# Kernel optimization log

Measured on AMD Instinct MI355X. Metric: run time of the kernel, lower is better.

Reference implementation:

```python
import jax, jax.numpy as jnp
import numpy as np
import math

EMBED = 1024
HEADS = 16
HEAD_DIM = EMBED // HEADS


def setup_inputs() -> dict:
    key = jax.random.key(0)
    ks = jax.random.split(key, 9)
    B, S = 2, 2048
    query = jax.random.normal(ks[0], (B, S, EMBED), dtype=jnp.float32)
    key_t = jax.random.normal(ks[1], (B, S, EMBED), dtype=jnp.float32)
    value = jax.random.normal(ks[2], (B, S, EMBED), dtype=jnp.float32)
    mask = jax.random.randint(ks[3], (B, 1, S, S), 0, 2, dtype=jnp.int32)
    # nn.Linear(head_dim, head_dim, bias=False) weights: [out, in]
    sc = 1.0 / math.sqrt(HEAD_DIM)
    Wq = jax.random.uniform(ks[4], (HEAD_DIM, HEAD_DIM), jnp.float32, -sc, sc)
    Wk = jax.random.uniform(ks[5], (HEAD_DIM, HEAD_DIM), jnp.float32, -sc, sc)
    Wv = jax.random.uniform(ks[6], (HEAD_DIM, HEAD_DIM), jnp.float32, -sc, sc)
    so = 1.0 / math.sqrt(EMBED)
    Wo = jax.random.uniform(ks[7], (EMBED, EMBED), jnp.float32, -so, so)
    bo = jax.random.uniform(ks[8], (EMBED,), jnp.float32, -so, so)
    return {"query": query, "key": key_t, "value": value, "mask": mask,
            "Wq": Wq, "Wk": Wk, "Wv": Wv, "Wo": Wo, "bo": bo}


def reference(query, key, value, mask, Wq, Wk, Wv, Wo, bo):
    B, Sq, E = query.shape
    Sk = key.shape[1]
    H, D = HEADS, HEAD_DIM
    # Faithful raw reshape into heads (as in the torch source, no transpose)
    q = query.reshape(B, H, Sq, D)
    k = key.reshape(B, H, Sk, D)
    v = value.reshape(B, H, Sk, D)
    # per-head_dim Linear (bias-free): x @ W.T
    Q = jnp.einsum('bhsd,ed->bhse', q, Wq)
    K = jnp.einsum('bhsd,ed->bhse', k, Wk)
    V = jnp.einsum('bhsd,ed->bhse', v, Wv)
    scores = jnp.einsum('bhqd,bhkd->bhqk', Q, K)  # [B,H,Sq,Sk]
    scores = jnp.where(mask == 0, jnp.float32(-1e20), scores)
    # NOTE: source divides by sqrt(embed_size), not sqrt(head_dim)
    attn = jax.nn.softmax(scores / jnp.float32(math.sqrt(E)), axis=-1)
    out = jnp.einsum('bhqk,bhkd->bhqd', attn, V).reshape(B, Sq, H * D)
    return out @ Wo.T + bo
```

## Files before the change

kernel.cpp:

```cpp
#include <hip/hip_runtime.h>

typedef __attribute__((ext_vector_type(8))) short short8;
typedef __attribute__((ext_vector_type(4))) float f32x4;
typedef __attribute__((ext_vector_type(2))) int int2v;
typedef __attribute__((ext_vector_type(4))) int int4v;

__device__ __forceinline__ short f2bf(float f) {
  unsigned u = __builtin_bit_cast(unsigned, f);
  u += 0x7fff + ((u >> 16) & 1);
  return (short)(u >> 16);
}

__device__ __forceinline__ int pk2bf(float lo, float hi) {
#if defined(__gfx950__) && __has_builtin(__builtin_amdgcn_cvt_pk_bf16_f32)
  typedef __attribute__((ext_vector_type(2))) __bf16 bf16x2;
  bf16x2 v = __builtin_amdgcn_cvt_pk_bf16_f32(lo, hi);
  return __builtin_bit_cast(int, v);
#else
  return (int)(unsigned short)(short)f2bf(lo) | (((int)f2bf(hi)) << 16);
#endif
}

__device__ __forceinline__ int pktr(float lo, float hi) {
  return (int)(__builtin_bit_cast(unsigned, lo) >> 16) |
         (int)(__builtin_bit_cast(unsigned, hi) & 0xffff0000u);
}

__device__ __forceinline__ short8 pack8(f32x4 a, f32x4 b) {
  int4v t;
  t.x = pk2bf(a[0], a[1]);
  t.y = pk2bf(a[2], a[3]);
  t.z = pk2bf(b[0], b[1]);
  t.w = pk2bf(b[2], b[3]);
  return __builtin_bit_cast(short8, t);
}

__device__ __forceinline__ float fand(float p, int m) {
  return __builtin_bit_cast(float, __builtin_bit_cast(int, p) & m);
}

__device__ __forceinline__ int bmask(unsigned w, int bit) {
#if __has_builtin(__builtin_amdgcn_sbfe)
  return __builtin_amdgcn_sbfe((int)w, bit, 1);
#else
  return ((int)(w << (31 - bit))) >> 31;
#endif
}

__device__ __forceinline__ float fexp2(float x) {
#if __has_builtin(__builtin_amdgcn_exp2f)
  return __builtin_amdgcn_exp2f(x);
#else
  return exp2f(x);
#endif
}

__device__ __forceinline__ void glds16(const short* g, short* lbase, int lane) {
#if __has_builtin(__builtin_amdgcn_global_load_lds)
  __builtin_amdgcn_global_load_lds(
      (const __attribute__((address_space(1))) unsigned int*)g,
      (__attribute__((address_space(3))) unsigned int*)lbase, 16, 0, 0);
#else
  *(short8*)(lbase + lane * 8) = *(const short8*)g;
#endif
}

__global__ __launch_bounds__(256) void prep(const float* __restrict__ q,
                                            const float* __restrict__ k,
                                            const float* __restrict__ v,
                                            const float* __restrict__ Wq,
                                            const float* __restrict__ Wk,
                                            const float* __restrict__ Wv,
                                            const float* __restrict__ Wo,
                                            const int* __restrict__ mask,
                                            short* __restrict__ Qp,
                                            short* __restrict__ Kp,
                                            short* __restrict__ Vtp,
                                            short* __restrict__ Wob,
                                            unsigned* __restrict__ mmod) {
  const int bid = blockIdx.x;
  const int tid = threadIdx.x;

  if (bid >= 4096) {
    const int mb = bid - 4096;
    const int kp = mb & 15, bq = mb >> 4;
    const int b_ = bq >> 5, q64 = bq & 31;
    const int wv = tid >> 6, qd = (tid >> 4) & 3, m16_ = tid & 15;
    unsigned d = 0;
#pragma unroll
    for (int hb = 0; hb < 2; ++hb) {
      const int ka = kp * 2 + hb;
#pragma unroll
      for (int r = 0; r < 4; ++r) {
        const int* mr = mask + b_ * 4194304 +
                        (q64 * 64 + wv * 16 + qd * 4 + r) * 2048 + ka * 64 + m16_;
#pragma unroll
        for (int nt = 0; nt < 4; ++nt)
          if (mr[nt * 16] != 0) d |= 1u << (hb * 16 + r * 4 + nt);
      }
    }
    mmod[mb * 256 + tid] = d;
    return;
  }
  if (bid >= 3072) {
    const int i = ((bid - 3072) * 256 + tid) * 4;
    const f32x4 x = *(const f32x4*)&Wo[i];
    int2v o;
    o.x = pk2bf(x[0], x[1]);
    o.y = pk2bf(x[2], x[3]);
    *(int2v*)&Wob[i] = o;
    return;
  }

  __shared__ short xt[64][72];
  __shared__ short ot[64][72];
  const int mode = bid >> 10;
  const int bt = bid & 1023;
  const float* X;
  const float* W;
  float scale;
  if (mode == 0) { X = q; W = Wq; scale = 0.045084220f; }
  else if (mode == 1) { X = k; W = Wk; scale = 1.0f; }
  else { X = v; W = Wv; scale = 1.0f; }

  const int r0 = bt * 64;
  const int row = tid >> 2, seg = (tid & 3) * 16;
  const f32x4* xs = (const f32x4*)(X + (r0 + row) * 64 + seg);
  const f32x4 x0 = xs[0], x1 = xs[1], x2 = xs[2], x3 = xs[3];
  *(short8*)&xt[row][seg] = pack8(x0, x1);
  *(short8*)&xt[row][seg + 8] = pack8(x2, x3);
  __syncthreads();

  const int lane = tid & 63, wave = tid >> 6;
  const int m16 = lane & 15, quad = lane >> 4;

  const short8 a0 = *(const short8*)&xt[wave * 16 + m16][quad * 8];
  const short8 a1 = *(const short8*)&xt[wave * 16 + m16][32 + quad * 8];

  f32x4 acc[4];
#pragma unroll
  for (int nt = 0; nt < 4; ++nt) {
    const f32x4* wp0 = (const f32x4*)&W[(nt * 16 + m16) * 64 + quad * 8];
    const f32x4* wp1 = (const f32x4*)&W[(nt * 16 + m16) * 64 + 32 + quad * 8];
    const short8 b0 = pack8(wp0[0], wp0[1]);
    const short8 b1 = pack8(wp1[0], wp1[1]);
    f32x4 z = (f32x4){0.f, 0.f, 0.f, 0.f};
    z = __builtin_amdgcn_mfma_f32_16x16x32_bf16(a0, b0, z, 0, 0, 0);
    z = __builtin_amdgcn_mfma_f32_16x16x32_bf16(a1, b1, z, 0, 0, 0);
    acc[nt] = z;
  }

  if (mode != 2) {
#pragma unroll
    for (int nt = 0; nt < 4; ++nt)
#pragma unroll
      for (int r = 0; r < 4; ++r)
        ot[wave * 16 + quad * 4 + r][nt * 16 + m16] = f2bf(acc[nt][r] * scale);
  } else {
#pragma unroll
    for (int nt = 0; nt < 4; ++nt)
#pragma unroll
      for (int r = 0; r < 4; ++r)
        ot[nt * 16 + m16][16 * quad + 4 * r + wave] = f2bf(acc[nt][r]);
  }
  __syncthreads();

  const int orow = tid >> 2, opart = tid & 3;
  if (mode != 2) {
    short* dst = (mode == 0 ? Qp : Kp) + (r0 + orow) * 64 + opart * 16;
    *(short8*)&dst[0] = *(const short8*)&ot[orow][opart * 16];
    *(short8*)&dst[8] = *(const short8*)&ot[orow][opart * 16 + 8];
  } else {
    const int bh = r0 >> 11, s0 = r0 & 2047;
    short* dst = Vtp + bh * 131072 + orow * 2048 + s0 + opart * 16;
    *(short8*)&dst[0] = *(const short8*)&ot[orow][opart * 16];
    *(short8*)&dst[8] = *(const short8*)&ot[orow][opart * 16 + 8];
  }
}

__global__ __launch_bounds__(256) void flash64f(const short* __restrict__ Qp,
                                                const short* __restrict__ Kp,
                                                const short* __restrict__ Vt,
                                                const unsigned* __restrict__ mmod,
                                                short* __restrict__ Ob) {
  __shared__ __attribute__((aligned(16))) short kt0[4096];
  __shared__ __attribute__((aligned(16))) short kt1[4096];
  __shared__ __attribute__((aligned(16))) short vt0[4096];
  __shared__ __attribute__((aligned(16))) short vt1[4096];
  __shared__ __attribute__((aligned(16))) short pt[4096];
  const int tid = threadIdx.x;
  const int bid = blockIdx.x;
  const int local = bid >> 3;
  const int qblk = local & 31;
  const int bh = (bid & 7) * 4 + (local >> 5);
  const int q0 = qblk << 6;
  const int b = bh >> 4;
  const short* Qh = Qp + bh * 131072;
  const short* Kh = Kp + bh * 131072;
  const short* Vh = Vt + bh * 131072;
  const int lane = tid & 63, wave = tid >> 6;
  const int m16 = lane & 15, quad = lane >> 4;
  const int srow = lane >> 3, sj = (lane & 7) ^ srow;
  const int koff = m16 * 128 + ((quad ^ (m16 & 7)) * 16);
  const unsigned* mq = mmod + ((b * 32 + qblk) * 16) * 256 + tid;

  char* const ptB = (char*)pt;
  int woff[4];
#pragma unroll
  for (int r = 0; r < 4; ++r)
    woff[r] = (wave * 16 + quad * 4 + r) * 128 +
              ((m16 * 8) ^ (((quad * 4 + r) & 7) << 4));
  const int aswz = (m16 & 7) << 4;
  const int aoff0 = (wave * 16 + m16) * 128 + ((quad * 16) ^ aswz);
  const int aoff1 = (wave * 16 + m16) * 128 + ((quad * 16 + 64) ^ aswz);

  short8 aq[2];
#pragma unroll
  for (int h = 0; h < 2; ++h)
    aq[h] = *(const short8*)&Qh[(q0 + wave * 16 + m16) * 64 + h * 32 + quad * 8];

  float l[4] = {0.f, 0.f, 0.f, 0.f};
  f32x4 oacc[4];
#pragma unroll
  for (int dt = 0; dt < 4; ++dt) oacc[dt] = (f32x4){0.f, 0.f, 0.f, 0.f};

  auto stage = [&](short* ktb, short* vtb, int ka) {
#pragma unroll
    for (int t = 0; t < 2; ++t) {
      const int crow = wave * 16 + t * 8;
      glds16(Kh + (ka * 64 + crow + srow) * 64 + sj * 8, ktb + crow * 64, lane);
      glds16(Vh + (crow + srow) * 2048 + ka * 64 + sj * 8, vtb + crow * 64, lane);
    }
  };

  auto compute = [&](const short* ktp, const short* vtp, unsigned mw, int bitbase) {
    const char* ktb = (const char*)ktp;
    const char* vtb = (const char*)vtp;
    f32x4 s[4];
    __builtin_amdgcn_s_setprio(1);
#pragma unroll
    for (int nt = 0; nt < 4; ++nt) {
      const int o0 = nt * 2048 + koff;
      const short8 kb0 = *(const short8*)(ktb + o0);
      const short8 kb1 = *(const short8*)(ktb + (o0 ^ 64));
      f32x4 z = (f32x4){0.f, 0.f, 0.f, 0.f};
      z = __builtin_amdgcn_mfma_f32_16x16x32_bf16(aq[0], kb0, z, 0, 0, 0);
      z = __builtin_amdgcn_mfma_f32_16x16x32_bf16(aq[1], kb1, z, 0, 0, 0);
      s[nt] = z;
    }
    __builtin_amdgcn_s_setprio(0);

#pragma unroll
    for (int r = 0; r < 4; ++r) {
      float p[4];
#pragma unroll
      for (int nt = 0; nt < 4; ++nt)
        p[nt] = fand(fexp2(s[nt][r]), bmask(mw, bitbase + r * 4 + nt));
      l[r] += (p[0] + p[1]) + (p[2] + p[3]);
      int2v pp;
      pp.x = pktr(p[0], p[1]);
      pp.y = pktr(p[2], p[3]);
      *(int2v*)(ptB + woff[r]) = pp;
    }

    const short8 ap0 = *(const short8*)(ptB + aoff0);
    const short8 ap1 = *(const short8*)(ptB + aoff1);
    __builtin_amdgcn_s_setprio(1);
#pragma unroll
    for (int dt = 0; dt < 4; ++dt) {
      const int o0 = dt * 2048 + koff;
      const short8 vb0 = *(const short8*)(vtb + o0);
      const short8 vb1 = *(const short8*)(vtb + (o0 ^ 64));
      f32x4 z = oacc[dt];
      z = __builtin_amdgcn_mfma_f32_16x16x32_bf16(ap0, vb0, z, 0, 0, 0);
      z = __builtin_amdgcn_mfma_f32_16x16x32_bf16(ap1, vb1, z, 0, 0, 0);
      oacc[dt] = z;
    }
    __builtin_amdgcn_s_setprio(0);
  };

  unsigned mw = mq[0];
  stage(kt0, vt0, 0);
  asm volatile("s_waitcnt vmcnt(0)" ::: "memory");
  __builtin_amdgcn_s_barrier();

  for (int kk = 0; kk < 16; ++kk) {
    stage(kt1, vt1, 2 * kk + 1);
    compute(kt0, vt0, mw, 0);
    asm volatile("s_waitcnt vmcnt(0)" ::: "memory");
    __builtin_amdgcn_s_barrier();

    unsigned mwn = 0u;
    if (kk < 15) {
      mwn = mq[(kk + 1) * 256];
      stage(kt0, vt0, 2 * kk + 2);
    }
    compute(kt1, vt1, mw, 16);
    mw = mwn;
    if (kk < 15) {
      asm volatile("s_waitcnt vmcnt(0)" ::: "memory");
      __builtin_amdgcn_s_barrier();
    }
  }

#pragma unroll
  for (int r = 0; r < 4; ++r) {
#pragma unroll
    for (int off = 1; off < 16; off <<= 1) l[r] += __shfl_xor(l[r], off, 16);
    const float inv = 1.0f / l[r];
#pragma unroll
    for (int dt = 0; dt < 4; ++dt)
      *(short*)(ptB + (wave * 16 + quad * 4 + r) * 128 +
                ((dt * 32 + m16 * 2) ^ (((quad * 4 + r) & 7) << 4))) =
          f2bf(oacc[dt][r] * inv);
  }

  const int orow = lane >> 2, opart = lane & 3;
  const int prow = wave * 16 + orow;
  const int oswz = (orow & 7) << 4;
  short* og = Ob + (bh * 2048 + q0 + prow) * 64 + opart * 16;
  *(short8*)&og[0] = *(const short8*)(ptB + prow * 128 + ((opart * 32) ^ oswz));
  *(short8*)&og[8] = *(const short8*)(ptB + prow * 128 + ((opart * 32 + 16) ^ oswz));
}

__global__ __launch_bounds__(256) void outproj(const short* __restrict__ Ob,
                                               const short* __restrict__ Wob,
                                               const float* __restrict__ bo,
                                               float* __restrict__ out) {
  __shared__ short at[64][72];
  __shared__ short bt[128][72];
  const int tid = threadIdx.x;
  const int bid = blockIdx.x;
  const int ct = bid >> 6, rt = bid & 63;
  const int r0 = rt * 64, c0 = ct * 128;
  const int lane = tid & 63, wave = tid >> 6;
  const int mr = (wave >> 1) * 32, nc = (wave & 1) * 64;
  const int m16 = lane & 15, quad = lane >> 4;
  const int arow = tid >> 2, apart = tid & 3;
  const int brow = tid >> 1, bhalf = (tid & 1) * 32;

  f32x4 acc[2][4];
#pragma unroll
  for (int mt = 0; mt < 2; ++mt)
#pragma unroll
    for (int nt = 0; nt < 4; ++nt) acc[mt][nt] = (f32x4){0.f, 0.f, 0.f, 0.f};

  for (int kc = 0; kc < 16; ++kc) {
    __syncthreads();
    const short* ag = &Ob[(r0 + arow) * 1024 + kc * 64 + apart * 16];
    const short* bg = &Wob[(c0 + brow) * 1024 + kc * 64 + bhalf];
    *(short8*)&at[arow][apart * 16] = *(const short8*)&ag[0];
    *(short8*)&at[arow][apart * 16 + 8] = *(const short8*)&ag[8];
    *(short8*)&bt[brow][bhalf] = *(const short8*)&bg[0];
    *(short8*)&bt[brow][bhalf + 8] = *(const short8*)&bg[8];
    *(short8*)&bt[brow][bhalf + 16] = *(const short8*)&bg[16];
    *(short8*)&bt[brow][bhalf + 24] = *(const short8*)&bg[24];
    __syncthreads();

#pragma unroll
    for (int kh = 0; kh < 2; ++kh) {
      short8 af[2], bf[4];
#pragma unroll
      for (int i = 0; i < 2; ++i)
        af[i] = *(const short8*)&at[mr + i * 16 + m16][kh * 32 + quad * 8];
#pragma unroll
      for (int j = 0; j < 4; ++j)
        bf[j] = *(const short8*)&bt[nc + j * 16 + m16][kh * 32 + quad * 8];
#pragma unroll
      for (int mt = 0; mt < 2; ++mt)
#pragma unroll
        for (int nt = 0; nt < 4; ++nt)
          acc[mt][nt] = __builtin_amdgcn_mfma_f32_16x16x32_bf16(af[mt], bf[nt], acc[mt][nt], 0, 0, 0);
    }
  }

#pragma unroll
  for (int nt = 0; nt < 4; ++nt) {
    const int col = c0 + nc + nt * 16 + m16;
    const float bias = bo[col];
#pragma unroll
    for (int mt = 0; mt < 2; ++mt)
#pragma unroll
      for (int rr2 = 0; rr2 < 4; ++rr2)
        out[(r0 + mr + mt * 16 + quad * 4 + rr2) * 1024 + col] = acc[mt][nt][rr2] + bias;
  }
}

extern "C" void kernel_launch(void* const* d_in, const int* in_sizes, int n_in,
                              void* d_out, int out_size, void* d_ws, size_t ws_size,
                              hipStream_t stream) {
  const float* query = (const float*)d_in[0];
  const float* key = (const float*)d_in[1];
  const float* value = (const float*)d_in[2];
  const int* mask = (const int*)d_in[3];
  const float* Wq = (const float*)d_in[4];
  const float* Wk = (const float*)d_in[5];
  const float* Wv = (const float*)d_in[6];
  const float* Wo = (const float*)d_in[7];
  const float* bo = (const float*)d_in[8];
  float* out = (float*)d_out;

  char* ws = (char*)d_ws;
  short* Qp = (short*)(ws);
  short* Kp = (short*)(ws + 8388608);
  short* Vt = (short*)(ws + 16777216);
  short* Ob = (short*)(ws + 25165824);
  short* Wob = (short*)(ws + 41943040);
  unsigned* mmod = (unsigned*)(ws + 44564480);

  prep<<<5120, 256, 0, stream>>>(query, key, value, Wq, Wk, Wv, Wo, mask,
                                 Qp, Kp, Vt, Wob, mmod);
  flash64f<<<1024, 256, 0, stream>>>(Qp, Kp, Vt, mmod, Ob);
  outproj<<<512, 256, 0, stream>>>(Ob, Wob, bo, out);
}
```

Measured before the change: 229.8 us.

## Process 128 query rows per flash block to reuse staged K/V tiles

The flash attention kernel now handles 128 query rows per workgroup (two 64-row halves per wave) instead of 64, halving the grid to 512 blocks. Each K/V tile staged into LDS therefore feeds twice as many MFMAs, which halves global K/V traffic and LDS staging per unit of work. The pipeline is also restructured: both buffers are prefetched up front and partial vmcnt waits replace full drains. In exchange, register pressure and LDS use rise, and only 512 blocks may underfill a 256-CU device.

```diff
diff --git a/kernel.cpp b/kernel.cpp
--- a/kernel.cpp
+++ b/kernel.cpp
@@ -178,7 +178,7 @@
   }
 }
 
-__global__ __launch_bounds__(256) void flash64f(const short* __restrict__ Qp,
+__global__ __launch_bounds__(256) void flash128(const short* __restrict__ Qp,
                                                 const short* __restrict__ Kp,
                                                 const short* __restrict__ Vt,
                                                 const unsigned* __restrict__ mmod,
@@ -187,13 +187,13 @@
   __shared__ __attribute__((aligned(16))) short kt1[4096];
   __shared__ __attribute__((aligned(16))) short vt0[4096];
   __shared__ __attribute__((aligned(16))) short vt1[4096];
-  __shared__ __attribute__((aligned(16))) short pt[4096];
+  __shared__ __attribute__((aligned(16))) short pt[8192];
   const int tid = threadIdx.x;
   const int bid = blockIdx.x;
   const int local = bid >> 3;
-  const int qblk = local & 31;
-  const int bh = (bid & 7) * 4 + (local >> 5);
-  const int q0 = qblk << 6;
+  const int qblk = local & 15;
+  const int bh = (bid & 7) * 4 + (local >> 4);
+  const int q0 = qblk << 7;
   const int b = bh >> 4;
   const short* Qh = Qp + bh * 131072;
   const short* Kh = Kp + bh * 131072;
@@ -202,27 +202,36 @@
   const int m16 = lane & 15, quad = lane >> 4;
   const int srow = lane >> 3, sj = (lane & 7) ^ srow;
   const int koff = m16 * 128 + ((quad ^ (m16 & 7)) * 16);
-  const unsigned* mq = mmod + ((b * 32 + qblk) * 16) * 256 + tid;
+  const unsigned* mqa = mmod + ((b * 32 + qblk * 2) * 16) * 256 + tid;
 
   char* const ptB = (char*)pt;
-  int woff[4];
-#pragma unroll
-  for (int r = 0; r < 4; ++r)
-    woff[r] = (wave * 16 + quad * 4 + r) * 128 +
-              ((m16 * 8) ^ (((quad * 4 + r) & 7) << 4));
+  int woff[2][4];
+  int aoff[2][2];
   const int aswz = (m16 & 7) << 4;
-  const int aoff0 = (wave * 16 + m16) * 128 + ((quad * 16) ^ aswz);
-  const int aoff1 = (wave * 16 + m16) * 128 + ((quad * 16 + 64) ^ aswz);
-
-  short8 aq[2];
-#pragma unroll
-  for (int h = 0; h < 2; ++h)
-    aq[h] = *(const short8*)&Qh[(q0 + wave * 16 + m16) * 64 + h * 32 + quad * 8];
-
-  float l[4] = {0.f, 0.f, 0.f, 0.f};
-  f32x4 oacc[4];
-#pragma unroll
-  for (int dt = 0; dt < 4; ++dt) oacc[dt] = (f32x4){0.f, 0.f, 0.f, 0.f};
+#pragma unroll
+  for (int mi = 0; mi < 2; ++mi) {
+#pragma unroll
+    for (int r = 0; r < 4; ++r)
+      woff[mi][r] = (mi * 64 + wave * 16 + quad * 4 + r) * 128 +
+                    ((m16 * 8) ^ (((quad * 4 + r) & 7) << 4));
+    aoff[mi][0] = (mi * 64 + wave * 16 + m16) * 128 + ((quad * 16) ^ aswz);
+    aoff[mi][1] = (mi * 64 + wave * 16 + m16) * 128 + (((quad * 16) + 64) ^ aswz);
+  }
+
+  short8 aq[2][2];
+#pragma unroll
+  for (int mi = 0; mi < 2; ++mi)
+#pragma unroll
+    for (int h = 0; h < 2; ++h)
+      aq[mi][h] = *(const short8*)&Qh[(q0 + mi * 64 + wave * 16 + m16) * 64 +
+                                      h * 32 + quad * 8];
+
+  float l[2][4] = {{0.f, 0.f, 0.f, 0.f}, {0.f, 0.f, 0.f, 0.f}};
+  f32x4 oacc[2][4];
+#pragma unroll
+  for (int mi = 0; mi < 2; ++mi)
+#pragma unroll
+    for (int dt = 0; dt < 4; ++dt) oacc[mi][dt] = (f32x4){0.f, 0.f, 0.f, 0.f};
 
   auto stage = [&](short* ktb, short* vtb, int ka) {
 #pragma unroll
@@ -233,94 +242,118 @@
     }
   };
 
-  auto compute = [&](const short* ktp, const short* vtp, unsigned mw, int bitbase) {
+  auto compute = [&](const short* ktp, const short* vtp, unsigned mwa, unsigned mwb,
+                     int bitbase) {
     const char* ktb = (const char*)ktp;
     const char* vtb = (const char*)vtp;
-    f32x4 s[4];
+    f32x4 s[2][4];
     __builtin_amdgcn_s_setprio(1);
 #pragma unroll
     for (int nt = 0; nt < 4; ++nt) {
       const int o0 = nt * 2048 + koff;
       const short8 kb0 = *(const short8*)(ktb + o0);
       const short8 kb1 = *(const short8*)(ktb + (o0 ^ 64));
-      f32x4 z = (f32x4){0.f, 0.f, 0.f, 0.f};
-      z = __builtin_amdgcn_mfma_f32_16x16x32_bf16(aq[0], kb0, z, 0, 0, 0);
-      z = __builtin_amdgcn_mfma_f32_16x16x32_bf16(aq[1], kb1, z, 0, 0, 0);
-      s[nt] = z;
+#pragma unroll
+      for (int mi = 0; mi < 2; ++mi) {
+        f32x4 z = (f32x4){0.f, 0.f, 0.f, 0.f};
+        z = __builtin_amdgcn_mfma_f32_16x16x32_bf16(aq[mi][0], kb0, z, 0, 0, 0);
+        z = __builtin_amdgcn_mfma_f32_16x16x32_bf16(aq[mi][1], kb1, z, 0, 0, 0);
+        s[mi][nt] = z;
+      }
     }
     __builtin_amdgcn_s_setprio(0);
 
 #pragma unroll
-    for (int r = 0; r < 4; ++r) {
-      float p[4];
-#pragma unroll
-      for (int nt = 0; nt < 4; ++nt)
-        p[nt] = fand(fexp2(s[nt][r]), bmask(mw, bitbase + r * 4 + nt));
-      l[r] += (p[0] + p[1]) + (p[2] + p[3]);
-      int2v pp;
-      pp.x = pktr(p[0], p[1]);
-      pp.y = pktr(p[2], p[3]);
-      *(int2v*)(ptB + woff[r]) = pp;
-    }
-
-    const short8 ap0 = *(const short8*)(ptB + aoff0);
-    const short8 ap1 = *(const short8*)(ptB + aoff1);
+    for (int mi = 0; mi < 2; ++mi) {
+      const unsigned mw = mi ? mwb : mwa;
+#pragma unroll
+      for (int r = 0; r < 4; ++r) {
+        float p[4];
+#pragma unroll
+        for (int nt = 0; nt < 4; ++nt)
+          p[nt] = fand(fexp2(s[mi][nt][r]), bmask(mw, bitbase + r * 4 + nt));
+        l[mi][r] += (p[0] + p[1]) + (p[2] + p[3]);
+        int2v pp;
+        pp.x = pktr(p[0], p[1]);
+        pp.y = pktr(p[2], p[3]);
+        *(int2v*)(ptB + woff[mi][r]) = pp;
+      }
+    }
+
+    short8 ap[2][2];
+#pragma unroll
+    for (int mi = 0; mi < 2; ++mi) {
+      ap[mi][0] = *(const short8*)(ptB + aoff[mi][0]);
+      ap[mi][1] = *(const short8*)(ptB + aoff[mi][1]);
+    }
     __builtin_amdgcn_s_setprio(1);
 #pragma unroll
     for (int dt = 0; dt < 4; ++dt) {
       const int o0 = dt * 2048 + koff;
       const short8 vb0 = *(const short8*)(vtb + o0);
       const short8 vb1 = *(const short8*)(vtb + (o0 ^ 64));
-      f32x4 z = oacc[dt];
-      z = __builtin_amdgcn_mfma_f32_16x16x32_bf16(ap0, vb0, z, 0, 0, 0);
-      z = __builtin_amdgcn_mfma_f32_16x16x32_bf16(ap1, vb1, z, 0, 0, 0);
-      oacc[dt] = z;
+#pragma unroll
+      for (int mi = 0; mi < 2; ++mi) {
+        f32x4 z = oacc[mi][dt];
+        z = __builtin_amdgcn_mfma_f32_16x16x32_bf16(ap[mi][0], vb0, z, 0, 0, 0);
+        z = __builtin_amdgcn_mfma_f32_16x16x32_bf16(ap[mi][1], vb1, z, 0, 0, 0);
+        oacc[mi][dt] = z;
+      }
     }
     __builtin_amdgcn_s_setprio(0);
   };
 
-  unsigned mw = mq[0];
+  unsigned mwa = mqa[0];
+  unsigned mwb = mqa[4096];
   stage(kt0, vt0, 0);
+  stage(kt1, vt1, 1);
+
+  for (int kk = 0; kk < 15; ++kk) {
+    const unsigned mwna = mqa[(kk + 1) * 256];
+    const unsigned mwnb = mqa[4096 + (kk + 1) * 256];
+    asm volatile("s_waitcnt vmcnt(6)" ::: "memory");
+    __builtin_amdgcn_s_barrier();
+    compute(kt0, vt0, mwa, mwb, 0);
+    __builtin_amdgcn_s_barrier();
+    stage(kt0, vt0, 2 * kk + 2);
+    asm volatile("s_waitcnt vmcnt(6)" ::: "memory");
+    __builtin_amdgcn_s_barrier();
+    compute(kt1, vt1, mwa, mwb, 16);
+    __builtin_amdgcn_s_barrier();
+    stage(kt1, vt1, 2 * kk + 3);
+    mwa = mwna;
+    mwb = mwnb;
+  }
+  asm volatile("s_waitcnt vmcnt(4)" ::: "memory");
+  __builtin_amdgcn_s_barrier();
+  compute(kt0, vt0, mwa, mwb, 0);
   asm volatile("s_waitcnt vmcnt(0)" ::: "memory");
   __builtin_amdgcn_s_barrier();
-
-  for (int kk = 0; kk < 16; ++kk) {
-    stage(kt1, vt1, 2 * kk + 1);
-    compute(kt0, vt0, mw, 0);
-    asm volatile("s_waitcnt vmcnt(0)" ::: "memory");
-    __builtin_amdgcn_s_barrier();
-
-    unsigned mwn = 0u;
-    if (kk < 15) {
-      mwn = mq[(kk + 1) * 256];
-      stage(kt0, vt0, 2 * kk + 2);
-    }
-    compute(kt1, vt1, mw, 16);
-    mw = mwn;
-    if (kk < 15) {
-      asm volatile("s_waitcnt vmcnt(0)" ::: "memory");
-      __builtin_amdgcn_s_barrier();
-    }
-  }
-
-#pragma unroll
-  for (int r = 0; r < 4; ++r) {
-#pragma unroll
-    for (int off = 1; off < 16; off <<= 1) l[r] += __shfl_xor(l[r], off, 16);
-    const float inv = 1.0f / l[r];
-#pragma unroll
-    for (int dt = 0; dt < 4; ++dt)
-      *(short*)(ptB + (wave * 16 + quad * 4 + r) * 128 +
-                ((dt * 32 + m16 * 2) ^ (((quad * 4 + r) & 7) << 4))) =
-          f2bf(oacc[dt][r] * inv);
-  }
+  compute(kt1, vt1, mwa, mwb, 16);
+
+#pragma unroll
+  for (int mi = 0; mi < 2; ++mi)
+#pragma unroll
+    for (int r = 0; r < 4; ++r) {
+#pragma unroll
+      for (int off = 1; off < 16; off <<= 1) l[mi][r] += __shfl_xor(l[mi][r], off, 16);
+      const float inv = 1.0f / l[mi][r];
+#pragma unroll
+      for (int dt = 0; dt < 4; ++dt)
+        *(short*)(ptB + (mi * 64 + wave * 16 + quad * 4 + r) * 128 +
+                  ((dt * 32 + m16 * 2) ^ (((quad * 4 + r) & 7) << 4))) =
+            f2bf(oacc[mi][dt][r] * inv);
+    }
 
   const int orow = lane >> 2, opart = lane & 3;
-  const int prow = wave * 16 + orow;
   const int oswz = (orow & 7) << 4;
-  short* og = Ob + (bh * 2048 + q0 + prow) * 64 + opart * 16;
-  *(short8*)&og[0] = *(const short8*)(ptB + prow * 128 + ((opart * 32) ^ oswz));
-  *(short8*)&og[8] = *(const short8*)(ptB + prow * 128 + ((opart * 32 + 16) ^ oswz));
+#pragma unroll
+  for (int mi = 0; mi < 2; ++mi) {
+    const int prow = mi * 64 + wave * 16 + orow;
+    short* og = Ob + (bh * 2048 + q0 + prow) * 64 + opart * 16;
+    *(short8*)&og[0] = *(const short8*)(ptB + prow * 128 + ((opart * 32) ^ oswz));
+    *(short8*)&og[8] = *(const short8*)(ptB + prow * 128 + ((opart * 32 + 16) ^ oswz));
+  }
 }
 
 __global__ __launch_bounds__(256) void outproj(const short* __restrict__ Ob,
@@ -410,6 +443,6 @@
 
   prep<<<5120, 256, 0, stream>>>(query, key, value, Wq, Wk, Wv, Wo, mask,
                                  Qp, Kp, Vt, Wob, mmod);
-  flash64f<<<1024, 256, 0, stream>>>(Qp, Kp, Vt, mmod, Ob);
+  flash128<<<512, 256, 0, stream>>>(Qp, Kp, Vt, mmod, Ob);
   outproj<<<512, 256, 0, stream>>>(Ob, Wob, bo, out);
 }
```

After: 246.2 us. 1.07x slower.

## Compute transposed scores to keep P in registers, drop LDS round-trip

Applied to the files above, without the earlier changes.

The QK^T MFMA now takes its operands in swapped order, so the score fragment lands in the register layout the PV MFMA expects. P is packed directly into A operands instead of being written to LDS and read back. To match, the V transpose layout and the mask bit layout in prep are permuted, and the row-sum reduction becomes cross-lane shuffles. The K/V double-buffer loop is also restructured with partial vmcnt waits, so loads for the next tile stay in flight during compute, at the cost of extra barriers.

```diff
diff --git a/kernel.cpp b/kernel.cpp
--- a/kernel.cpp
+++ b/kernel.cpp
@@ -89,15 +89,13 @@
     unsigned d = 0;
 #pragma unroll
     for (int hb = 0; hb < 2; ++hb) {
-      const int ka = kp * 2 + hb;
-#pragma unroll
-      for (int r = 0; r < 4; ++r) {
-        const int* mr = mask + b_ * 4194304 +
-                        (q64 * 64 + wv * 16 + qd * 4 + r) * 2048 + ka * 64 + m16_;
-#pragma unroll
-        for (int nt = 0; nt < 4; ++nt)
-          if (mr[nt * 16] != 0) d |= 1u << (hb * 16 + r * 4 + nt);
-      }
+      const int* mr = mask + b_ * 4194304 + (q64 * 64 + wv * 16 + m16_) * 2048 +
+                      (kp * 2 + hb) * 64 + qd * 4;
+#pragma unroll
+      for (int grp = 0; grp < 4; ++grp)
+#pragma unroll
+        for (int r = 0; r < 4; ++r)
+          if (mr[grp * 16 + r] != 0) d |= 1u << (hb * 16 + grp * 4 + r);
     }
     mmod[mb * 256 + tid] = d;
     return;
@@ -161,7 +159,8 @@
     for (int nt = 0; nt < 4; ++nt)
 #pragma unroll
       for (int r = 0; r < 4; ++r)
-        ot[nt * 16 + m16][16 * quad + 4 * r + wave] = f2bf(acc[nt][r]);
+        ot[nt * 16 + m16][quad * 8 + (wave & 1) * 4 + r + (wave >> 1) * 32] =
+            f2bf(acc[nt][r]);
   }
   __syncthreads();
 
@@ -178,7 +177,7 @@
   }
 }
 
-__global__ __launch_bounds__(256) void flash64f(const short* __restrict__ Qp,
+__global__ __launch_bounds__(256) void flash64r(const short* __restrict__ Qp,
                                                 const short* __restrict__ Kp,
                                                 const short* __restrict__ Vt,
                                                 const unsigned* __restrict__ mmod,
@@ -202,24 +201,16 @@
   const int m16 = lane & 15, quad = lane >> 4;
   const int srow = lane >> 3, sj = (lane & 7) ^ srow;
   const int koff = m16 * 128 + ((quad ^ (m16 & 7)) * 16);
-  const unsigned* mq = mmod + ((b * 32 + qblk) * 16) * 256 + tid;
+  const unsigned* mq = mmod + ((b * 32 + qblk) * 16) * 256 + wave * 64 + quad * 16 + m16;
 
   char* const ptB = (char*)pt;
-  int woff[4];
-#pragma unroll
-  for (int r = 0; r < 4; ++r)
-    woff[r] = (wave * 16 + quad * 4 + r) * 128 +
-              ((m16 * 8) ^ (((quad * 4 + r) & 7) << 4));
-  const int aswz = (m16 & 7) << 4;
-  const int aoff0 = (wave * 16 + m16) * 128 + ((quad * 16) ^ aswz);
-  const int aoff1 = (wave * 16 + m16) * 128 + ((quad * 16 + 64) ^ aswz);
 
   short8 aq[2];
 #pragma unroll
   for (int h = 0; h < 2; ++h)
     aq[h] = *(const short8*)&Qh[(q0 + wave * 16 + m16) * 64 + h * 32 + quad * 8];
 
-  float l[4] = {0.f, 0.f, 0.f, 0.f};
+  float l = 0.f;
   f32x4 oacc[4];
 #pragma unroll
   for (int dt = 0; dt < 4; ++dt) oacc[dt] = (f32x4){0.f, 0.f, 0.f, 0.f};
@@ -233,38 +224,47 @@
     }
   };
 
-  auto compute = [&](const short* ktp, const short* vtp, unsigned mw, int bitbase) {
+  auto compute = [&](const short* ktp, const short* vtp, unsigned mw, int bb) {
     const char* ktb = (const char*)ktp;
     const char* vtb = (const char*)vtp;
     f32x4 s[4];
     __builtin_amdgcn_s_setprio(1);
 #pragma unroll
-    for (int nt = 0; nt < 4; ++nt) {
-      const int o0 = nt * 2048 + koff;
+    for (int grp = 0; grp < 4; ++grp) {
+      const int o0 = grp * 2048 + koff;
       const short8 kb0 = *(const short8*)(ktb + o0);
       const short8 kb1 = *(const short8*)(ktb + (o0 ^ 64));
       f32x4 z = (f32x4){0.f, 0.f, 0.f, 0.f};
-      z = __builtin_amdgcn_mfma_f32_16x16x32_bf16(aq[0], kb0, z, 0, 0, 0);
-      z = __builtin_amdgcn_mfma_f32_16x16x32_bf16(aq[1], kb1, z, 0, 0, 0);
-      s[nt] = z;
+      z = __builtin_amdgcn_mfma_f32_16x16x32_bf16(kb0, aq[0], z, 0, 0, 0);
+      z = __builtin_amdgcn_mfma_f32_16x16x32_bf16(kb1, aq[1], z, 0, 0, 0);
+      s[grp] = z;
     }
     __builtin_amdgcn_s_setprio(0);
 
-#pragma unroll
-    for (int r = 0; r < 4; ++r) {
-      float p[4];
-#pragma unroll
-      for (int nt = 0; nt < 4; ++nt)
-        p[nt] = fand(fexp2(s[nt][r]), bmask(mw, bitbase + r * 4 + nt));
-      l[r] += (p[0] + p[1]) + (p[2] + p[3]);
-      int2v pp;
-      pp.x = pktr(p[0], p[1]);
-      pp.y = pktr(p[2], p[3]);
-      *(int2v*)(ptB + woff[r]) = pp;
-    }
-
-    const short8 ap0 = *(const short8*)(ptB + aoff0);
-    const short8 ap1 = *(const short8*)(ptB + aoff1);
+    float p[4][4];
+#pragma unroll
+    for (int grp = 0; grp < 4; ++grp)
+#pragma unroll
+      for (int r = 0; r < 4; ++r)
+        p[grp][r] = fand(fexp2(s[grp][r]), bmask(mw, bb + grp * 4 + r));
+    float g0 = (p[0][0] + p[0][1]) + (p[0][2] + p[0][3]);
+    float g1 = (p[1][0] + p[1][1]) + (p[1][2] + p[1][3]);
+    float g2 = (p[2][0] + p[2][1]) + (p[2][2] + p[2][3]);
+    float g3 = (p[3][0] + p[3][1]) + (p[3][2] + p[3][3]);
+    l += (g0 + g1) + (g2 + g3);
+
+    int4v t0, t1;
+    t0.x = pktr(p[0][0], p[0][1]);
+    t0.y = pktr(p[0][2], p[0][3]);
+    t0.z = pktr(p[1][0], p[1][1]);
+    t0.w = pktr(p[1][2], p[1][3]);
+    t1.x = pktr(p[2][0], p[2][1]);
+    t1.y = pktr(p[2][2], p[2][3]);
+    t1.z = pktr(p[3][0], p[3][1]);
+    t1.w = pktr(p[3][2], p[3][3]);
+    const short8 ap0 = __builtin_bit_cast(short8, t0);
+    const short8 ap1 = __builtin_bit_cast(short8, t1);
+
     __builtin_amdgcn_s_setprio(1);
 #pragma unroll
     for (int dt = 0; dt < 4; ++dt) {
@@ -281,39 +281,44 @@
 
   unsigned mw = mq[0];
   stage(kt0, vt0, 0);
+  stage(kt1, vt1, 1);
+
+  for (int kk = 0; kk < 15; ++kk) {
+    const unsigned mwn = mq[(kk + 1) * 256];
+    asm volatile("s_waitcnt vmcnt(5)" ::: "memory");
+    __builtin_amdgcn_s_barrier();
+    compute(kt0, vt0, mw, 0);
+    __builtin_amdgcn_s_barrier();
+    stage(kt0, vt0, 2 * kk + 2);
+    asm volatile("s_waitcnt vmcnt(5)" ::: "memory");
+    __builtin_amdgcn_s_barrier();
+    compute(kt1, vt1, mw, 16);
+    __builtin_amdgcn_s_barrier();
+    stage(kt1, vt1, 2 * kk + 3);
+    mw = mwn;
+  }
+  asm volatile("s_waitcnt vmcnt(4)" ::: "memory");
+  __builtin_amdgcn_s_barrier();
+  compute(kt0, vt0, mw, 0);
   asm volatile("s_waitcnt vmcnt(0)" ::: "memory");
   __builtin_amdgcn_s_barrier();
-
-  for (int kk = 0; kk < 16; ++kk) {
-    stage(kt1, vt1, 2 * kk + 1);
-    compute(kt0, vt0, mw, 0);
-    asm volatile("s_waitcnt vmcnt(0)" ::: "memory");
-    __builtin_amdgcn_s_barrier();
-
-    unsigned mwn = 0u;
-    if (kk < 15) {
-      mwn = mq[(kk + 1) * 256];
-      stage(kt0, vt0, 2 * kk + 2);
-    }
-    compute(kt1, vt1, mw, 16);
-    mw = mwn;
-    if (kk < 15) {
-      asm volatile("s_waitcnt vmcnt(0)" ::: "memory");
-      __builtin_amdgcn_s_barrier();
-    }
-  }
+  compute(kt1, vt1, mw, 16);
+
+  l += __shfl_xor(l, 16);
+  l += __shfl_xor(l, 32);
+  float linv[4];
+#pragma unroll
+  for (int r = 0; r < 4; ++r) linv[r] = 1.0f / __shfl(l, quad * 4 + r, 64);
 
 #pragma unroll
   for (int r = 0; r < 4; ++r) {
-#pragma unroll
-    for (int off = 1; off < 16; off <<= 1) l[r] += __shfl_xor(l[r], off, 16);
-    const float inv = 1.0f / l[r];
+    const int row = wave * 16 + quad * 4 + r;
 #pragma unroll
     for (int dt = 0; dt < 4; ++dt)
-      *(short*)(ptB + (wave * 16 + quad * 4 + r) * 128 +
-                ((dt * 32 + m16 * 2) ^ (((quad * 4 + r) & 7) << 4))) =
-          f2bf(oacc[dt][r] * inv);
-  }
+      *(short*)(ptB + row * 128 + ((dt * 32 + m16 * 2) ^ ((row & 7) << 4))) =
+          f2bf(oacc[dt][r] * linv[r]);
+  }
+  asm volatile("s_waitcnt lgkmcnt(0)" ::: "memory");
 
   const int orow = lane >> 2, opart = lane & 3;
   const int prow = wave * 16 + orow;
@@ -410,6 +415,6 @@
 
   prep<<<5120, 256, 0, stream>>>(query, key, value, Wq, Wk, Wv, Wo, mask,
                                  Qp, Kp, Vt, Wob, mmod);
-  flash64f<<<1024, 256, 0, stream>>>(Qp, Kp, Vt, mmod, Ob);
+  flash64r<<<1024, 256, 0, stream>>>(Qp, Kp, Vt, mmod, Ob);
   outproj<<<512, 256, 0, stream>>>(Ob, Wob, bo, out);
 }
```

New measurement: 220.2 us. 4.2% less time.
